# Kernel optimization log

Measured on AMD Instinct MI355X. Metric: run time of the kernel, lower is better.

The kernel has to match this reference:

```python
import jax, jax.numpy as jnp
import numpy as np

THRESHOLD = 0.5
EPS = 1e-6


def setup_inputs() -> dict:
    key = jax.random.key(0)
    k1, k2 = jax.random.split(key)
    points = jax.random.normal(k1, (16, 10, 30, 2), dtype=jnp.float32)
    polys = jax.random.normal(k2, (16, 16, 200, 2), dtype=jnp.float32)
    return {"points": points, "drivable_multipolygon": polys}


def reference(points, drivable_multipolygon):
    # points: (B, C, T, 2); drivable_multipolygon: (B, K, N, 2)
    # Broadcast layout: (B, K, C, T, N-1, ...)
    ps = drivable_multipolygon[:, :, None, None, :-1, :]   # edge starts (B,K,1,1,N-1,2)
    pe = drivable_multipolygon[:, :, None, None, 1:, :]    # edge ends   (B,K,1,1,N-1,2)
    pts = points[:, None, :, :, None, :]                   # (B,1,C,T,1,2)

    # --- point-to-segment distance ---
    v1 = pts - ps
    ev = pe - ps
    dot = jnp.sum(v1 * ev, axis=-1)
    esq = jnp.sum(ev * ev, axis=-1)
    proj = jnp.clip(dot / (esq + EPS), 0.0, 1.0)
    closest = ev * proj[..., None] + ps
    dist_sq = jnp.maximum(jnp.sum((pts - closest) ** 2, axis=-1), EPS)
    min_dist = jnp.min(jnp.sqrt(dist_sq), axis=-1)         # min over edges N-1 -> (B,K,C,T)
    min_dist = jnp.min(min_dist, axis=1)                   # min over polygons K -> (B,C,T)

    # --- ray-casting inside test (parity of crossings) ---
    py = pts[..., 1]
    px = pts[..., 0]
    sy, sx = ps[..., 1], ps[..., 0]
    ey, ex = pe[..., 1], pe[..., 0]
    cond_y = ((sy <= py) & (py < ey)) | ((ey <= py) & (py < sy))
    slope = (ey - sy) / (ex - sx + EPS)
    intersect_x = sx + (py - sy) / (slope + EPS)
    is_left = intersect_x > px
    intersection = cond_y & is_left                        # (B,K,C,T,N-1)
    crossings = jnp.sum(jnp.sum(intersection.astype(jnp.int32), axis=-1), axis=1)  # (B,C,T)
    inside = (crossings % 2) == 1

    min_dist = jnp.where(inside, -min_dist, min_dist)
    min_dist = jax.nn.relu(min_dist + THRESHOLD)
    return jnp.sum(min_dist, axis=-1)                      # (B, C)
```

## Files before the change

kernel.cpp:

```cpp
#include <hip/hip_runtime.h>
#include <math.h>
#include <float.h>

#define EPS 1e-6f
#define THRESHOLD 0.5f

#define NB 16
#define NPOLY 16
#define NVERT 200
#define NSEG_PER_POLY 199
#define NSEG (NPOLY * NSEG_PER_POLY)
#define NPTB 300
#define NPOINTS 4800
#define NSLICE 64
#define SEG_PER_SLICE 50

__global__ __launch_bounds__(320) void seg_kernel(
    const float* __restrict__ points,
    const float* __restrict__ polys,
    float2* __restrict__ part,
    float* __restrict__ out)
{
    __shared__ float4 lds[SEG_PER_SLICE * 2];

    const int slice = blockIdx.x;
    const int b     = blockIdx.y;
    const int lp    = threadIdx.x;
    const bool active = lp < NPTB;

    const int s0 = slice * SEG_PER_SLICE;
    const int s1 = (s0 + SEG_PER_SLICE < NSEG) ? s0 + SEG_PER_SLICE : NSEG;
    const int nseg = s1 - s0;

    if (lp < nseg) {
        const int s = s0 + lp;
        const int m = s / NSEG_PER_POLY;
        const int v = s % NSEG_PER_POLY;
        const float2* poly = (const float2*)polys + ((size_t)(b * NPOLY + m) * NVERT);
        const float2 S = poly[v];
        const float2 E = poly[v + 1];
        const float evx = E.x - S.x;
        const float evy = E.y - S.y;
        const float esq = evx * evx + evy * evy;
        const float inv_esq = 1.0f / (esq + EPS);
        const float slope_eps = evy / (evx + EPS) + EPS;
        const float inv_slope = __builtin_amdgcn_rcpf(slope_eps);
        lds[lp * 2]     = make_float4(S.x, S.y, evx, evy);
        lds[lp * 2 + 1] = make_float4(inv_esq, slope_eps, inv_slope, E.y);
    }
    __syncthreads();

    const int pidx = b * NPTB + (active ? lp : 0);
    const float2 pt = *(const float2*)(points + (size_t)pidx * 2);
    const float px = pt.x, py = pt.y;

    float min_a = FLT_MAX, min_b = FLT_MAX;
    int cr_a = 0, cr_b = 0;

    auto body = [&](int j, float& mn, int& cr) {
        const float4 p0 = lds[j * 2];
        const float4 p1 = lds[j * 2 + 1];
        const float sx = p0.x, sy = p0.y, evx = p0.z, evy = p0.w;
        const float inv_esq = p1.x, slope_eps = p1.y, inv_slope = p1.z, ey = p1.w;

        const float v1x = px - sx;
        const float v1y = py - sy;
        const float dot = fmaf(v1y, evy, v1x * evx);
        const float t   = __builtin_amdgcn_fmed3f(dot * inv_esq, 0.0f, 1.0f);
        const float dx  = fmaf(-evx, t, v1x);
        const float dy  = fmaf(-evy, t, v1y);
        const float dsq = fmaf(dy, dy, dx * dx);
        mn = fminf(mn, dsq);

        const bool cond_y = (sy <= py) != (ey <= py);
        const float q    = v1y * inv_slope;
        const float ixa  = sx + q;
        const float diff = ixa - px;
        const float err  = fmaf(fabsf(q) + fabsf(ixa), 1e-6f, 1e-30f);
        bool left = diff > 0.0f;
        if (cond_y && !(fabsf(diff) > err)) {
            left = (sx + v1y / slope_eps) > px;
        }
        cr += (cond_y && left) ? 1 : 0;
    };

    for (int j = 0; j < nseg; j += 2) {
        body(j,     min_a, cr_a);
        body(j + 1, min_b, cr_b);
    }

    if (active) {
        part[slice * NPOINTS + pidx] =
            make_float2(fminf(min_a, min_b), __int_as_float(cr_a + cr_b));
    } else if (slice == 0 && lp >= NPTB && lp < NPTB + 10) {
        out[b * 10 + (lp - NPTB)] = 0.0f;
    }
}

__global__ __launch_bounds__(256) void final_kernel(
    const float2* __restrict__ part,
    float* __restrict__ out)
{
    const int p = blockIdx.x * 256 + threadIdx.x;
    if (p >= NPOINTS) return;

    float md = FLT_MAX;
    int c = 0;
    #pragma unroll 8
    for (int k = 0; k < NSLICE; ++k) {
        const float2 pr = part[k * NPOINTS + p];
        md = fminf(md, pr.x);
        c += __float_as_int(pr.y);
    }

    float d = sqrtf(fmaxf(md, EPS));
    if (c & 1) d = -d;
    const float val = fmaxf(d + THRESHOLD, 0.0f);

    const int b = p / NPTB;
    const int a = (p % NPTB) / 30;
    atomicAdd(out + b * 10 + a, val);
}

extern "C" void kernel_launch(void* const* d_in, const int* in_sizes, int n_in,
                              void* d_out, int out_size, void* d_ws, size_t ws_size,
                              hipStream_t stream) {
    const float* points = (const float*)d_in[0];
    const float* polys  = (const float*)d_in[1];
    float* out = (float*)d_out;

    float2* part = (float2*)d_ws;

    dim3 grid(NSLICE, NB);
    seg_kernel<<<grid, 320, 0, stream>>>(points, polys, part, out);
    final_kernel<<<(NPOINTS + 255) / 256, 256, 0, stream>>>(part, out);
}
```

Before: 80.30 us.

## Precompute padded segment table in separate kernel; read uniformly from global in seg kernel

Adds a precompute kernel that builds a padded per-batch table of segment parameters (3200 entries, padded with dummy segments that never count as crossings). The main kernel drops its LDS staging and barrier and reads the table from global memory with wave-uniform addresses, and its loop now has a fixed trip count. The aim is to remove per-block redundant setup and the sync stall. The cost is an extra kernel launch and table traffic through global memory and cache in place of LDS.

```diff
diff --git a/kernel.cpp b/kernel.cpp
--- a/kernel.cpp
+++ b/kernel.cpp
@@ -9,82 +9,94 @@
 #define NPOLY 16
 #define NVERT 200
 #define NSEG_PER_POLY 199
-#define NSEG (NPOLY * NSEG_PER_POLY)
+#define NSEG_REAL (NPOLY * NSEG_PER_POLY)
+#define NSEG_PAD 3200
 #define NPTB 300
 #define NPOINTS 4800
 #define NSLICE 64
 #define SEG_PER_SLICE 50
 
+struct __align__(32) Seg {
+    float sx, sy, evx, evy, inv_esq, slope_eps, inv_slope, ey;
+};
+
+__global__ __launch_bounds__(256) void precompute_kernel(
+    const float* __restrict__ polys,
+    Seg* __restrict__ table,
+    float* __restrict__ out)
+{
+    const int idx = blockIdx.x * 256 + threadIdx.x;
+    if (idx < 160) out[idx] = 0.0f;
+
+    const int b = idx / NSEG_PAD;
+    const int s = idx % NSEG_PAD;
+
+    Seg e;
+    if (s < NSEG_REAL) {
+        const int m = s / NSEG_PER_POLY;
+        const int v = s % NSEG_PER_POLY;
+        const float2* poly = (const float2*)polys + ((size_t)(b * NPOLY + m) * NVERT);
+        const float2 S = poly[v];
+        const float2 E = poly[v + 1];
+        e.sx = S.x; e.sy = S.y;
+        e.evx = E.x - S.x;
+        e.evy = E.y - S.y;
+        const float esq = e.evx * e.evx + e.evy * e.evy;
+        e.inv_esq   = 1.0f / (esq + EPS);
+        e.slope_eps = e.evy / (e.evx + EPS) + EPS;
+        e.inv_slope = __builtin_amdgcn_rcpf(e.slope_eps);
+        e.ey = E.y;
+    } else {
+        e.sx = 1e30f; e.sy = 1e30f; e.evx = 0.0f; e.evy = 0.0f;
+        e.inv_esq = 0.0f; e.slope_eps = 1.0f; e.inv_slope = 1.0f; e.ey = 1e30f;
+    }
+    table[idx] = e;
+}
+
 __global__ __launch_bounds__(320) void seg_kernel(
     const float* __restrict__ points,
-    const float* __restrict__ polys,
-    float2* __restrict__ part,
-    float* __restrict__ out)
+    const Seg* __restrict__ table,
+    float2* __restrict__ part)
 {
-    __shared__ float4 lds[SEG_PER_SLICE * 2];
-
     const int slice = blockIdx.x;
     const int b     = blockIdx.y;
     const int lp    = threadIdx.x;
     const bool active = lp < NPTB;
 
-    const int s0 = slice * SEG_PER_SLICE;
-    const int s1 = (s0 + SEG_PER_SLICE < NSEG) ? s0 + SEG_PER_SLICE : NSEG;
-    const int nseg = s1 - s0;
-
-    if (lp < nseg) {
-        const int s = s0 + lp;
-        const int m = s / NSEG_PER_POLY;
-        const int v = s % NSEG_PER_POLY;
-        const float2* poly = (const float2*)polys + ((size_t)(b * NPOLY + m) * NVERT);
-        const float2 S = poly[v];
-        const float2 E = poly[v + 1];
-        const float evx = E.x - S.x;
-        const float evy = E.y - S.y;
-        const float esq = evx * evx + evy * evy;
-        const float inv_esq = 1.0f / (esq + EPS);
-        const float slope_eps = evy / (evx + EPS) + EPS;
-        const float inv_slope = __builtin_amdgcn_rcpf(slope_eps);
-        lds[lp * 2]     = make_float4(S.x, S.y, evx, evy);
-        lds[lp * 2 + 1] = make_float4(inv_esq, slope_eps, inv_slope, E.y);
-    }
-    __syncthreads();
-
     const int pidx = b * NPTB + (active ? lp : 0);
     const float2 pt = *(const float2*)(points + (size_t)pidx * 2);
     const float px = pt.x, py = pt.y;
+
+    const Seg* __restrict__ tb = table + (b * NSEG_PAD + slice * SEG_PER_SLICE);
 
     float min_a = FLT_MAX, min_b = FLT_MAX;
     int cr_a = 0, cr_b = 0;
 
     auto body = [&](int j, float& mn, int& cr) {
-        const float4 p0 = lds[j * 2];
-        const float4 p1 = lds[j * 2 + 1];
-        const float sx = p0.x, sy = p0.y, evx = p0.z, evy = p0.w;
-        const float inv_esq = p1.x, slope_eps = p1.y, inv_slope = p1.z, ey = p1.w;
+        const Seg sg = tb[j];
 
-        const float v1x = px - sx;
-        const float v1y = py - sy;
-        const float dot = fmaf(v1y, evy, v1x * evx);
-        const float t   = __builtin_amdgcn_fmed3f(dot * inv_esq, 0.0f, 1.0f);
-        const float dx  = fmaf(-evx, t, v1x);
-        const float dy  = fmaf(-evy, t, v1y);
+        const float v1x = px - sg.sx;
+        const float v1y = py - sg.sy;
+        const float dot = fmaf(v1y, sg.evy, v1x * sg.evx);
+        const float t   = __builtin_amdgcn_fmed3f(dot * sg.inv_esq, 0.0f, 1.0f);
+        const float dx  = fmaf(-sg.evx, t, v1x);
+        const float dy  = fmaf(-sg.evy, t, v1y);
         const float dsq = fmaf(dy, dy, dx * dx);
         mn = fminf(mn, dsq);
 
-        const bool cond_y = (sy <= py) != (ey <= py);
-        const float q    = v1y * inv_slope;
-        const float ixa  = sx + q;
+        const bool cond_y = (sg.sy <= py) != (sg.ey <= py);
+        const float q    = v1y * sg.inv_slope;
+        const float ixa  = sg.sx + q;
         const float diff = ixa - px;
         const float err  = fmaf(fabsf(q) + fabsf(ixa), 1e-6f, 1e-30f);
         bool left = diff > 0.0f;
         if (cond_y && !(fabsf(diff) > err)) {
-            left = (sx + v1y / slope_eps) > px;
+            left = (sg.sx + v1y / sg.slope_eps) > px;
         }
         cr += (cond_y && left) ? 1 : 0;
     };
 
-    for (int j = 0; j < nseg; j += 2) {
+    for (int j = 0; j < SEG_PER_SLICE; j += 2) {
         body(j,     min_a, cr_a);
         body(j + 1, min_b, cr_b);
     }
@@ -92,8 +104,6 @@
     if (active) {
         part[slice * NPOINTS + pidx] =
             make_float2(fminf(min_a, min_b), __int_as_float(cr_a + cr_b));
-    } else if (slice == 0 && lp >= NPTB && lp < NPTB + 10) {
-        out[b * 10 + (lp - NPTB)] = 0.0f;
     }
 }
 
@@ -129,9 +139,14 @@
     const float* polys  = (const float*)d_in[1];
     float* out = (float*)d_out;
 
-    float2* part = (float2*)d_ws;
+    char* ws = (char*)d_ws;
+    Seg*    table = (Seg*)ws;
+    float2* part  = (float2*)(ws + (2u << 20));
+
+    precompute_kernel<<<NB * NSEG_PAD / 256, 256, 0, stream>>>(polys, table, out);
 
     dim3 grid(NSLICE, NB);
-    seg_kernel<<<grid, 320, 0, stream>>>(points, polys, part, out);
+    seg_kernel<<<grid, 320, 0, stream>>>(points, table, part);
+
     final_kernel<<<(NPOINTS + 255) / 256, 256, 0, stream>>>(part, out);
 }
```

After: 85.54 us. +6.5%, slower.
